# Kernel tuning notes

Hardware: AMD Instinct MI355X
Metric: run time of the kernel (lower is better)

## Reference

```python
import jax, jax.numpy as jnp
import numpy as np

B, TK, NK, H = 64, 512, 256, 512

def _masked_renorm_softmax(scores, mask):
    # softmax over last dim, multiply by mask, renormalize (as in the torch code)
    p = jax.nn.softmax(scores, axis=-1) * mask
    return p / jnp.sum(p, axis=-1, keepdims=True)

def setup_inputs() -> dict:
    key = jax.random.key(0)
    ks = jax.random.split(key, 14)
    s = 0.02
    return {
        "s_t_hat": jax.random.normal(ks[0], (B, 2 * H), jnp.float32),
        "encoder_outputs_token": jax.random.normal(ks[1], (B, TK, H), jnp.float32),
        "encoder_outputs_node": jax.random.normal(ks[2], (B, NK, H), jnp.float32),
        "node_to_token": jax.random.randint(ks[3], (B, TK), 0, NK),
        "enc_padding_mask_token": jnp.ones((B, TK), jnp.float32),
        "enc_padding_mask_node": jnp.ones((B, NK), jnp.float32),
        "graph": jax.random.uniform(ks[4], (B, NK, NK), jnp.float32),
        "flow": jax.random.uniform(ks[5], (B, NK), jnp.float32),
        # parameters (Linear weights stored as [in, out]; x @ W == torch Linear)
        "W_c": jax.random.normal(ks[6], (H,), jnp.float32) * s,          # Linear(1, H)
        "W_tok": jax.random.normal(ks[7], (H, H), jnp.float32) * s,      # encode_proj_token
        "W_node": jax.random.normal(ks[8], (H, H), jnp.float32) * s,     # encode_proj_node
        "W_dec": jax.random.normal(ks[9], (2 * H, H), jnp.float32) * s,  # decode_proj
        "b_dec": jnp.zeros((H,), jnp.float32),
        "v_tok": jax.random.normal(ks[10], (H,), jnp.float32) * s,       # v_token
        "v_node": jax.random.normal(ks[11], (H,), jnp.float32) * s,      # v_node
    }

def reference(s_t_hat, encoder_outputs_token, encoder_outputs_node, node_to_token,
              enc_padding_mask_token, enc_padding_mask_node, graph, flow,
              W_c, W_tok, W_node, W_dec, b_dec, v_tok, v_node):
    # projections
    enc_tok_feat = jnp.einsum('bth,hk->btk', encoder_outputs_token, W_tok)   # [B,TK,H]
    enc_node_feat = jnp.einsum('bnh,hk->bnk', encoder_outputs_node, W_node)  # [B,NK,H]
    dec_fea = s_t_hat @ W_dec + b_dec                                        # [B,H]
    flow_feat = flow[..., None] * W_c                                        # [B,NK,H]

    # node attention
    e_node = jnp.tanh(enc_node_feat + dec_fea[:, None, :] + flow_feat)
    scores_node = jnp.einsum('bnh,h->bn', e_node, v_node)                    # [B,NK]
    attn_dist_node = _masked_renorm_softmax(scores_node, enc_padding_mask_node)

    # gather node attention onto tokens via node_to_token indices
    gathered = jnp.take_along_axis(attn_dist_node, node_to_token, axis=1)    # [B,TK]
    attn_dist_node_to_token = _masked_renorm_softmax(gathered, enc_padding_mask_token)

    # token attention
    e_tok = jnp.tanh(enc_tok_feat + dec_fea[:, None, :])
    scores_tok = jnp.einsum('bth,h->bt', e_tok, v_tok)                       # [B,TK]
    attn_dist_token = _masked_renorm_softmax(scores_tok, enc_padding_mask_token)

    # mix and context
    final_attn = 0.5 * attn_dist_token + 0.5 * attn_dist_node_to_token      # [B,TK]
    c_t = jnp.einsum('bt,bth->bh', final_attn, encoder_outputs_token)        # [B,H]

    # multi-hop graph diffusion of node attention
    zero_hop = attn_dist_node                                                # [B,NK]
    one_hop = jnp.einsum('bn,bnm->bm', zero_hop, graph)
    two_hop = jnp.einsum('bn,bnm->bm', one_hop, graph)
    flow_out = (zero_hop + one_hop + two_hop) * 0.33333

    return (c_t, final_attn, attn_dist_node, flow_out)
```

## Files before the change

### kernel.cpp

```cpp
#include <hip/hip_runtime.h>
#include <math.h>

constexpr int kB = 64;
constexpr int kTK = 512;
constexpr int kNK = 256;
constexpr int kH = 512;
constexpr int kTokBlocks = kB * kTK / 64;
constexpr int kNodeBlocks = kB * kNK / 64;

typedef float f32x4 __attribute__((ext_vector_type(4)));
typedef __bf16 bf16x8 __attribute__((ext_vector_type(8)));

__device__ __forceinline__ unsigned short f32_to_bf16(float f) {
  return (unsigned short)((__float_as_uint(f) + 0x8000u) >> 16);
}

__device__ __forceinline__ float tanh_fast(float x) {
  float e = __builtin_amdgcn_exp2f(x * 2.8853900817779268f);
  return 1.0f - 2.0f * __builtin_amdgcn_rcpf(e + 1.0f);
}

__device__ __forceinline__ void lds_barrier() {
  __builtin_amdgcn_s_waitcnt(0xC07F);
  __builtin_amdgcn_s_barrier();
}

__device__ __forceinline__ void gload_lds16(const void* g, void* l) {
  __builtin_amdgcn_global_load_lds(
      (__attribute__((address_space(1))) void*)(g),
      (__attribute__((address_space(3))) void*)(l), 16, 0, 0);
}

__global__ __launch_bounds__(256) void prep_kernel(
    const float* __restrict__ Wtok, const float* __restrict__ Wnode,
    unsigned short* __restrict__ WtokT, unsigned short* __restrict__ WnodeT,
    const float* __restrict__ s_t_hat, const float* __restrict__ W_dec,
    float* __restrict__ dec_part) {
  __shared__ float sm[32 * 33];
  const int tid = threadIdx.x;
  if (blockIdx.x < 512) {
    const int idx = blockIdx.x;
    const int z = idx >> 8, rem = idx & 255;
    const int bx = rem & 15, by = rem >> 4;
    const float* W = z ? Wnode : Wtok;
    unsigned short* T = z ? WnodeT : WtokT;
    const int tx = tid & 31, ty = tid >> 5;
#pragma unroll
    for (int i = 0; i < 4; ++i)
      sm[(ty + 8 * i) * 33 + tx] =
          W[(size_t)(by * 32 + ty + 8 * i) * kH + bx * 32 + tx];
    __syncthreads();
#pragma unroll
    for (int i = 0; i < 4; ++i)
      T[(size_t)(bx * 32 + ty + 8 * i) * kH + by * 32 + tx] =
          f32_to_bf16(sm[tx * 33 + ty + 8 * i]);
  } else {
    const int r = blockIdx.x - 512;
    const int b = r >> 3, s = r & 7;
    if (tid < 128) sm[tid] = s_t_hat[(size_t)b * 1024 + s * 128 + tid];
    __syncthreads();
    float a0 = 0.f, a1 = 0.f;
    const float* w = W_dec + (size_t)(s * 128) * kH;
#pragma unroll 8
    for (int k = 0; k < 128; ++k) {
      a0 = fmaf(sm[k], w[(size_t)k * kH + tid], a0);
      a1 = fmaf(sm[k], w[(size_t)k * kH + tid + 256], a1);
    }
    dec_part[(size_t)(b * 8 + s) * kH + tid] = a0;
    dec_part[(size_t)(b * 8 + s) * kH + tid + 256] = a1;
  }
}

__global__ __launch_bounds__(512, 4) void scores_fused_kernel(
    const float* __restrict__ enc_tok, const float* __restrict__ enc_node,
    const unsigned short* __restrict__ WtokT,
    const unsigned short* __restrict__ WnodeT,
    const float* __restrict__ dec_part, const float* __restrict__ b_dec,
    const float* __restrict__ flow, const float* __restrict__ W_c,
    const float* __restrict__ v_tok, const float* __restrict__ v_node,
    float* __restrict__ scores_tok, float* __restrict__ scores_node) {
  const int tid = threadIdx.x;
  const int wave = tid >> 6, lane = tid & 63;
  const int quad = lane >> 4, l15 = lane & 15;
  const bool is_node = blockIdx.x >= kTokBlocks;
  const int bidx = is_node ? (int)blockIdx.x - kTokBlocks : (int)blockIdx.x;
  const float* A = is_node ? enc_node : enc_tok;
  const unsigned short* WT = is_node ? WnodeT : WtokT;
  const float* v = is_node ? v_node : v_tok;
  float* scores = is_node ? scores_node : scores_tok;
  const int ROWS = is_node ? kNK : kTK;
  const int b = is_node ? (bidx >> 2) : (bidx >> 3);
  const int row0 = (is_node ? (bidx & 3) : (bidx & 7)) * 64;

  __shared__ __align__(16) float fbuf[2][4096];
  __shared__ __align__(16) unsigned short hbuf[2][4096];
  __shared__ float red[8][64];

  const f32x4 fzero = {0.f, 0.f, 0.f, 0.f};
  f32x4 acc[4][4];
#pragma unroll
  for (int i = 0; i < 4; ++i)
#pragma unroll
    for (int j = 0; j < 4; ++j) acc[i][j] = fzero;

  const float* asrcw =
      A + (size_t)(b * ROWS + row0 + wave * 8 + (lane >> 4)) * kH + (lane & 15) * 4;
  auto stage = [&](int kc, int buf) {
    gload_lds16(asrcw + kc * 64, &fbuf[buf][(wave * 8) * 64]);
    gload_lds16(asrcw + 4 * kH + kc * 64, &fbuf[buf][(wave * 8 + 4) * 64]);
  };

  auto cvt = [&](int buf) {
#pragma unroll
    for (int j = 0; j < 2; ++j) {
      const int e0 = j * 2048 + tid * 4;
      const int row = e0 >> 6, k = e0 & 63;
      const f32x4 x = *(const f32x4*)&fbuf[buf][e0];
      ushort4 h;
      h.x = f32_to_bf16(x[0]); h.y = f32_to_bf16(x[1]);
      h.z = f32_to_bf16(x[2]); h.w = f32_to_bf16(x[3]);
      const int s16 = (k >> 3) ^ (row & 7);
      *(ushort4*)((char*)&hbuf[buf][0] + row * 128 + s16 * 16 + (k & 7) * 2) = h;
    }
  };

  auto readfrag = [&](int buf, int ks, int mi) {
    const int row = mi * 16 + l15;
    const int s16 = (ks * 4 + quad) ^ (row & 7);
    return *(const bf16x8*)((const char*)&hbuf[buf][0] + row * 128 + s16 * 16);
  };

  const int n0 = wave * 64;
  const unsigned short* bbase = WT + (size_t)(n0 + l15) * kH + quad * 8;
  bf16x8 bbuf[2][2];
  auto loadB = [&](int sb, int g, int half) {
    bbuf[sb][0] = *(const bf16x8*)(bbase + (size_t)(16 * (2 * half + 0)) * kH + g * 32);
    bbuf[sb][1] = *(const bf16x8*)(bbase + (size_t)(16 * (2 * half + 1)) * kH + g * 32);
  };

  stage(0, 0);
  loadB(0, 0, 0);
  loadB(1, 0, 1);

#pragma unroll
  for (int kc = 0; kc < 8; ++kc) {
    __builtin_amdgcn_s_waitcnt(0x0F70);
    __builtin_amdgcn_sched_barrier(0);
    cvt(kc & 1);
    if (kc < 7) stage(kc + 1, (kc + 1) & 1);
    lds_barrier();
#pragma unroll
    for (int ks = 0; ks < 2; ++ks) {
      const int g = kc * 2 + ks;
      bf16x8 afr[4];
#pragma unroll
      for (int mi = 0; mi < 4; ++mi) afr[mi] = readfrag(kc & 1, ks, mi);
      if (g > 0) loadB(1, g, 1);
      __builtin_amdgcn_s_setprio(1);
#pragma unroll
      for (int mi = 0; mi < 4; ++mi)
#pragma unroll
        for (int ni = 0; ni < 2; ++ni)
          acc[mi][ni] = __builtin_amdgcn_mfma_f32_16x16x32_bf16(
              afr[mi], bbuf[0][ni], acc[mi][ni], 0, 0, 0);
      __builtin_amdgcn_s_setprio(0);
      if (g < 15) loadB(0, g + 1, 0);
      __builtin_amdgcn_s_setprio(1);
#pragma unroll
      for (int mi = 0; mi < 4; ++mi)
#pragma unroll
        for (int ni = 0; ni < 2; ++ni)
          acc[mi][ni + 2] = __builtin_amdgcn_mfma_f32_16x16x32_bf16(
              afr[mi], bbuf[1][ni], acc[mi][ni + 2], 0, 0, 0);
      __builtin_amdgcn_s_setprio(0);
    }
  }

  float dec2[4], vv2[4], wc2[4];
#pragma unroll
  for (int ni = 0; ni < 4; ++ni) {
    const int col = n0 + 16 * ni + l15;
    float d = b_dec[col];
#pragma unroll
    for (int p = 0; p < 8; ++p) d += dec_part[(size_t)(b * 8 + p) * kH + col];
    dec2[ni] = d;
    vv2[ni] = v[col];
    wc2[ni] = is_node ? W_c[col] : 0.f;
  }
#pragma unroll
  for (int mi = 0; mi < 4; ++mi) {
#pragma unroll
    for (int reg = 0; reg < 4; ++reg) {
      const int row = 16 * mi + quad * 4 + reg;
      const float fl = is_node ? flow[b * kNK + row0 + row] : 0.f;
      float p = 0.f;
#pragma unroll
      for (int ni = 0; ni < 4; ++ni)
        p += tanh_fast(fmaf(fl, wc2[ni], acc[mi][ni][reg] + dec2[ni])) * vv2[ni];
#pragma unroll
      for (int off = 1; off < 16; off <<= 1) p += __shfl_xor(p, off, 64);
      if (l15 == 0) red[wave][row] = p;
    }
  }
  __syncthreads();
  if (tid < 64) {
    float s = 0.f;
#pragma unroll
    for (int w = 0; w < 8; ++w) s += red[w][tid];
    scores[b * ROWS + row0 + tid] = s;
  }
}

__device__ __forceinline__ float block_sum_512(float v, float* rbuf) {
#pragma unroll
  for (int off = 32; off >= 1; off >>= 1) v += __shfl_xor(v, off, 64);
  if ((threadIdx.x & 63) == 0) rbuf[threadIdx.x >> 6] = v;
  __syncthreads();
  float s = rbuf[0];
#pragma unroll
  for (int w = 1; w < 8; ++w) s += rbuf[w];
  __syncthreads();
  return s;
}

__global__ __launch_bounds__(512) void softmax_mix_kernel(
    const float* __restrict__ scores_node, const float* __restrict__ scores_tok,
    const int* __restrict__ node_to_token,
    const float* __restrict__ mask_tok, const float* __restrict__ mask_node,
    float* __restrict__ out_final, float* __restrict__ out_attn_node,
    float* __restrict__ out_flow) {
  const int b = blockIdx.x, tid = threadIdx.x;
  __shared__ float an_sh[kNK];
  __shared__ float rbuf[8];

  if (tid < kNK) out_flow[b * kNK + tid] = 0.f;

  float en = 0.f;
  if (tid < kNK)
    en = expf(scores_node[b * kNK + tid]) * mask_node[b * kNK + tid];
  float sn = block_sum_512(en, rbuf);
  float an = en / sn;
  if (tid < kNK) {
    an_sh[tid] = an;
    out_attn_node[b * kNK + tid] = an;
  }
  __syncthreads();

  const float mt = mask_tok[b * kTK + tid];
  const int idx = node_to_token[b * kTK + tid];
  float eg = expf(an_sh[idx]) * mt;
  float sg = block_sum_512(eg, rbuf);
  float an2t = eg / sg;

  float et = expf(scores_tok[b * kTK + tid]) * mt;
  float st = block_sum_512(et, rbuf);
  float at = et / st;

  out_final[b * kTK + tid] = 0.5f * (at + an2t);
}

__global__ __launch_bounds__(512) void ct_flow1_kernel(
    const float* __restrict__ final_attn, const float* __restrict__ enc_tok,
    const float* __restrict__ attn_node, const float* __restrict__ graph,
    float* __restrict__ ctp, float* __restrict__ fp1) {
  const int tid = threadIdx.x;
  if (blockIdx.x < 512) {
    const int b = blockIdx.x >> 3, s = blockIdx.x & 7;
    __shared__ float fa[64];
    __shared__ float part[4][512];
    if (tid < 64) fa[tid] = final_attn[b * kTK + s * 64 + tid];
    __syncthreads();
    const int h4 = (tid & 127) * 4, tsub = tid >> 7;
    float4 acc = {0.f, 0.f, 0.f, 0.f};
    const float* base =
        enc_tok + ((size_t)(b * kTK + s * 64 + tsub * 16)) * kH + h4;
#pragma unroll
    for (int t = 0; t < 16; ++t) {
      float4 e = *(const float4*)(base + (size_t)t * kH);
      const float w = fa[tsub * 16 + t];
      acc.x = fmaf(w, e.x, acc.x); acc.y = fmaf(w, e.y, acc.y);
      acc.z = fmaf(w, e.z, acc.z); acc.w = fmaf(w, e.w, acc.w);
    }
    *(float4*)&part[tsub][h4] = acc;
    __syncthreads();
    if (tid < 128) {
      float4 s0 = {0.f, 0.f, 0.f, 0.f};
#pragma unroll
      for (int p = 0; p < 4; ++p) {
        float4 pp = *(const float4*)&part[p][tid * 4];
        s0.x += pp.x; s0.y += pp.y; s0.z += pp.z; s0.w += pp.w;
      }
      *(float4*)&ctp[((size_t)(b * 8 + s)) * kH + tid * 4] = s0;
    }
  } else {
    const int rr = blockIdx.x - 512;
    const int b = rr >> 2, sl = rr & 3;
    __shared__ float z[64];
    __shared__ float part[8][256];
    if (tid < 64) z[tid] = attn_node[b * kNK + sl * 64 + tid];
    __syncthreads();
    const int m4 = (tid & 63) * 4, nsub = tid >> 6;
    float4 acc = {0.f, 0.f, 0.f, 0.f};
    const float* g =
        graph + ((size_t)(b * kNK + sl * 64 + nsub * 8)) * kNK + m4;
#pragma unroll
    for (int n = 0; n < 8; ++n) {
      float4 gg = *(const float4*)(g + (size_t)n * kNK);
      const float w = z[nsub * 8 + n];
      acc.x = fmaf(w, gg.x, acc.x); acc.y = fmaf(w, gg.y, acc.y);
      acc.z = fmaf(w, gg.z, acc.z); acc.w = fmaf(w, gg.w, acc.w);
    }
    *(float4*)&part[nsub][m4] = acc;
    __syncthreads();
    if (tid < 64) {
      float4 s0 = {0.f, 0.f, 0.f, 0.f};
#pragma unroll
      for (int p = 0; p < 8; ++p) {
        float4 pp = *(const float4*)&part[p][tid * 4];
        s0.x += pp.x; s0.y += pp.y; s0.z += pp.z; s0.w += pp.w;
      }
      *(float4*)&fp1[((size_t)(b * 4 + sl)) * kNK + tid * 4] = s0;
    }
  }
}

__global__ __launch_bounds__(512) void ct_flow2_kernel(
    const float* __restrict__ ctp, const float* __restrict__ fp1,
    const float* __restrict__ attn_node, const float* __restrict__ graph,
    float* __restrict__ out_ct, float* __restrict__ out_flow) {
  const int tid = threadIdx.x;
  if (blockIdx.x < 64) {
    const int b = blockIdx.x;
    __shared__ float acc_sh[4][512];
    const int h4 = (tid & 127) * 4, part = tid >> 7;
    float4 a = {0.f, 0.f, 0.f, 0.f};
#pragma unroll
    for (int j = 0; j < 2; ++j) {
      float4 c = *(const float4*)&ctp[((size_t)(b * 8 + part * 2 + j)) * kH + h4];
      a.x += c.x; a.y += c.y; a.z += c.z; a.w += c.w;
    }
    *(float4*)&acc_sh[part][h4] = a;
    __syncthreads();
    if (tid < 128) {
      float4 s = {0.f, 0.f, 0.f, 0.f};
#pragma unroll
      for (int p = 0; p < 4; ++p) {
        float4 pp = *(const float4*)&acc_sh[p][tid * 4];
        s.x += pp.x; s.y += pp.y; s.z += pp.z; s.w += pp.w;
      }
      *(float4*)&out_ct[b * kH + tid * 4] = s;
    }
  } else {
    const int rr = blockIdx.x - 64;
    const int b = rr >> 2, sl = rr & 3;
    __shared__ float one_sh[64];
    __shared__ float part2[8][256];
    if (tid < 64) {
      const int n = sl * 64 + tid;
      float one = 0.f;
#pragma unroll
      for (int p = 0; p < 4; ++p) one += fp1[((size_t)(b * 4 + p)) * kNK + n];
      one_sh[tid] = one;
      atomicAdd(&out_flow[b * kNK + n],
                (attn_node[b * kNK + n] + one) * 0.33333f);
    }
    __syncthreads();
    const int m4 = (tid & 63) * 4, nsub = tid >> 6;
    float4 acc = {0.f, 0.f, 0.f, 0.f};
    const float* g =
        graph + ((size_t)(b * kNK + sl * 64 + nsub * 8)) * kNK + m4;
#pragma unroll
    for (int n = 0; n < 8; ++n) {
      float4 gg = *(const float4*)(g + (size_t)n * kNK);
      const float w = one_sh[sl * 0 + nsub * 8 + n];
      acc.x = fmaf(w, gg.x, acc.x); acc.y = fmaf(w, gg.y, acc.y);
      acc.z = fmaf(w, gg.z, acc.z); acc.w = fmaf(w, gg.w, acc.w);
    }
    *(float4*)&part2[nsub][m4] = acc;
    __syncthreads();
    if (tid < 64) {
      float4 s = {0.f, 0.f, 0.f, 0.f};
#pragma unroll
      for (int p = 0; p < 8; ++p) {
        float4 pp = *(const float4*)&part2[p][tid * 4];
        s.x += pp.x; s.y += pp.y; s.z += pp.z; s.w += pp.w;
      }
      float* dst = &out_flow[b * kNK + tid * 4];
      atomicAdd(dst + 0, s.x * 0.33333f);
      atomicAdd(dst + 1, s.y * 0.33333f);
      atomicAdd(dst + 2, s.z * 0.33333f);
      atomicAdd(dst + 3, s.w * 0.33333f);
    }
  }
}

extern "C" void kernel_launch(void* const* d_in, const int* in_sizes, int n_in,
                              void* d_out, int out_size, void* d_ws, size_t ws_size,
                              hipStream_t stream) {
  (void)in_sizes; (void)n_in; (void)out_size; (void)ws_size;
  const float* s_t_hat  = (const float*)d_in[0];
  const float* enc_tok  = (const float*)d_in[1];
  const float* enc_node = (const float*)d_in[2];
  const int*   n2t      = (const int*)d_in[3];
  const float* mask_tok = (const float*)d_in[4];
  const float* mask_nd  = (const float*)d_in[5];
  const float* graph    = (const float*)d_in[6];
  const float* flow     = (const float*)d_in[7];
  const float* W_c      = (const float*)d_in[8];
  const float* W_tok    = (const float*)d_in[9];
  const float* W_node   = (const float*)d_in[10];
  const float* W_dec    = (const float*)d_in[11];
  const float* b_dec    = (const float*)d_in[12];
  const float* v_tok    = (const float*)d_in[13];
  const float* v_node   = (const float*)d_in[14];

  float* out = (float*)d_out;
  float* out_ct        = out;
  float* out_final     = out + kB * kH;
  float* out_attn_node = out + 2 * kB * kH;
  float* out_flow      = out_attn_node + kB * kNK;

  float* ws = (float*)d_ws;
  float* scores_tok  = ws;
  float* scores_node = ws + 32768;
  float* dec_part    = ws + 49152;
  float* ctp         = dec_part;
  float* fp1         = ws + 311296;
  unsigned short* WtokT  = (unsigned short*)(ws + 376832);
  unsigned short* WnodeT = WtokT + kH * kH;

  prep_kernel<<<1024, 256, 0, stream>>>(W_tok, W_node, WtokT, WnodeT,
                                        s_t_hat, W_dec, dec_part);
  scores_fused_kernel<<<kTokBlocks + kNodeBlocks, 512, 0, stream>>>(
      enc_tok, enc_node, WtokT, WnodeT, dec_part, b_dec, flow, W_c,
      v_tok, v_node, scores_tok, scores_node);
  softmax_mix_kernel<<<kB, 512, 0, stream>>>(scores_node, scores_tok, n2t,
                                             mask_tok, mask_nd, out_final,
                                             out_attn_node, out_flow);
  ct_flow1_kernel<<<768, 512, 0, stream>>>(out_final, enc_tok, out_attn_node,
                                           graph, ctp, fp1);
  ct_flow2_kernel<<<320, 512, 0, stream>>>(ctp, fp1, out_attn_node, graph,
                                           out_ct, out_flow);
}
```

Baseline: 235.9 us.

## Split scores GEMM across two column-half blocks with partial score sums

The fused scores kernel now launches twice as many 256-thread blocks, each covering half of the output columns (256 of 512) for a 64-row tile. Each block writes a partial score into a separate half of an enlarged scores buffer, and the softmax kernel adds the two partials before exponentiating. This raises block count and parallelism across CUs, and gives each wave 16 rows of the A staging instead of 8. The cost is that every A tile is loaded and converted to bf16 twice, and the workspace layout shifts to fit the doubled score buffers.

```diff
diff --git a/kernel.cpp b/kernel.cpp
--- a/kernel.cpp
+++ b/kernel.cpp
@@ -5,8 +5,6 @@
 constexpr int kTK = 512;
 constexpr int kNK = 256;
 constexpr int kH = 512;
-constexpr int kTokBlocks = kB * kTK / 64;
-constexpr int kNodeBlocks = kB * kNK / 64;
 
 typedef float f32x4 __attribute__((ext_vector_type(4)));
 typedef __bf16 bf16x8 __attribute__((ext_vector_type(8)));
@@ -71,7 +69,7 @@
   }
 }
 
-__global__ __launch_bounds__(512, 4) void scores_fused_kernel(
+__global__ __launch_bounds__(256, 3) void scores_fused_kernel(
     const float* __restrict__ enc_tok, const float* __restrict__ enc_node,
     const unsigned short* __restrict__ WtokT,
     const unsigned short* __restrict__ WnodeT,
@@ -82,19 +80,22 @@
   const int tid = threadIdx.x;
   const int wave = tid >> 6, lane = tid & 63;
   const int quad = lane >> 4, l15 = lane & 15;
-  const bool is_node = blockIdx.x >= kTokBlocks;
-  const int bidx = is_node ? (int)blockIdx.x - kTokBlocks : (int)blockIdx.x;
+  const bool is_node = blockIdx.x >= 1024;
+  int bx = is_node ? (int)blockIdx.x - 1024 : (int)blockIdx.x;
+  const int colhalf = bx & 1;
+  bx >>= 1;
   const float* A = is_node ? enc_node : enc_tok;
   const unsigned short* WT = is_node ? WnodeT : WtokT;
   const float* v = is_node ? v_node : v_tok;
-  float* scores = is_node ? scores_node : scores_tok;
   const int ROWS = is_node ? kNK : kTK;
-  const int b = is_node ? (bidx >> 2) : (bidx >> 3);
-  const int row0 = (is_node ? (bidx & 3) : (bidx & 7)) * 64;
+  const int b = is_node ? (bx >> 2) : (bx >> 3);
+  const int row0 = (is_node ? (bx & 3) : (bx & 7)) * 64;
+  float* scores = (is_node ? scores_node : scores_tok) +
+                  (size_t)colhalf * (kB * ROWS);
 
   __shared__ __align__(16) float fbuf[2][4096];
   __shared__ __align__(16) unsigned short hbuf[2][4096];
-  __shared__ float red[8][64];
+  __shared__ float red[4][64];
 
   const f32x4 fzero = {0.f, 0.f, 0.f, 0.f};
   f32x4 acc[4][4];
@@ -104,16 +105,18 @@
     for (int j = 0; j < 4; ++j) acc[i][j] = fzero;
 
   const float* asrcw =
-      A + (size_t)(b * ROWS + row0 + wave * 8 + (lane >> 4)) * kH + (lane & 15) * 4;
+      A + (size_t)(b * ROWS + row0 + wave * 16 + (lane >> 4)) * kH + (lane & 15) * 4;
   auto stage = [&](int kc, int buf) {
-    gload_lds16(asrcw + kc * 64, &fbuf[buf][(wave * 8) * 64]);
-    gload_lds16(asrcw + 4 * kH + kc * 64, &fbuf[buf][(wave * 8 + 4) * 64]);
+#pragma unroll
+    for (int j = 0; j < 4; ++j)
+      gload_lds16(asrcw + (size_t)(4 * j) * kH + kc * 64,
+                  &fbuf[buf][(wave * 16 + 4 * j) * 64]);
   };
 
   auto cvt = [&](int buf) {
 #pragma unroll
-    for (int j = 0; j < 2; ++j) {
-      const int e0 = j * 2048 + tid * 4;
+    for (int j = 0; j < 4; ++j) {
+      const int e0 = j * 1024 + tid * 4;
       const int row = e0 >> 6, k = e0 & 63;
       const f32x4 x = *(const f32x4*)&fbuf[buf][e0];
       ushort4 h;
@@ -130,7 +133,7 @@
     return *(const bf16x8*)((const char*)&hbuf[buf][0] + row * 128 + s16 * 16);
   };
 
-  const int n0 = wave * 64;
+  const int n0 = colhalf * 256 + wave * 64;
   const unsigned short* bbase = WT + (size_t)(n0 + l15) * kH + quad * 8;
   bf16x8 bbuf[2][2];
   auto loadB = [&](int sb, int g, int half) {
@@ -206,7 +209,7 @@
   if (tid < 64) {
     float s = 0.f;
 #pragma unroll
-    for (int w = 0; w < 8; ++w) s += red[w][tid];
+    for (int w = 0; w < 4; ++w) s += red[w][tid];
     scores[b * ROWS + row0 + tid] = s;
   }
 }
@@ -236,8 +239,11 @@
   if (tid < kNK) out_flow[b * kNK + tid] = 0.f;
 
   float en = 0.f;
-  if (tid < kNK)
-    en = expf(scores_node[b * kNK + tid]) * mask_node[b * kNK + tid];
+  if (tid < kNK) {
+    const float s2 = scores_node[b * kNK + tid] +
+                     scores_node[kB * kNK + b * kNK + tid];
+    en = expf(s2) * mask_node[b * kNK + tid];
+  }
   float sn = block_sum_512(en, rbuf);
   float an = en / sn;
   if (tid < kNK) {
@@ -252,7 +258,9 @@
   float sg = block_sum_512(eg, rbuf);
   float an2t = eg / sg;
 
-  float et = expf(scores_tok[b * kTK + tid]) * mt;
+  const float st2 = scores_tok[b * kTK + tid] +
+                    scores_tok[kB * kTK + b * kTK + tid];
+  float et = expf(st2) * mt;
   float st = block_sum_512(et, rbuf);
   float at = et / st;
 
@@ -422,16 +430,16 @@
 
   float* ws = (float*)d_ws;
   float* scores_tok  = ws;
-  float* scores_node = ws + 32768;
-  float* dec_part    = ws + 49152;
+  float* scores_node = ws + 65536;
+  float* dec_part    = ws + 98304;
   float* ctp         = dec_part;
-  float* fp1         = ws + 311296;
-  unsigned short* WtokT  = (unsigned short*)(ws + 376832);
+  float* fp1         = ws + 360448;
+  unsigned short* WtokT  = (unsigned short*)(ws + 425984);
   unsigned short* WnodeT = WtokT + kH * kH;
 
   prep_kernel<<<1024, 256, 0, stream>>>(W_tok, W_node, WtokT, WnodeT,
                                         s_t_hat, W_dec, dec_part);
-  scores_fused_kernel<<<kTokBlocks + kNodeBlocks, 512, 0, stream>>>(
+  scores_fused_kernel<<<1536, 256, 0, stream>>>(
       enc_tok, enc_node, WtokT, WnodeT, dec_part, b_dec, flow, W_c,
       v_tok, v_node, scores_tok, scores_node);
   softmax_mix_kernel<<<kB, 512, 0, stream>>>(scores_node, scores_tok, n2t,
```

Result: no change. 239.5 us (+1.5%).

## Triple-buffer A staging and burst-load B fragments per K chunk

Applied to the files above, without the earlier changes.

Raises the fp32 LDS staging of the A tile from double to triple buffering, so global-to-LDS loads are issued two chunks ahead and the wait keeps two loads in flight. The B weight fragments for a whole K chunk (8 fragments) are now loaded in one burst before the barrier instead of being interleaved between MFMA halves. The fp32-to-bf16 conversion is remapped so each thread converts 8 contiguous values and writes one 16-byte packed store. LDS use and register pressure both grow, so launch bounds drop from 4 to 3 blocks per CU, trading occupancy for deeper prefetch.

```diff
diff --git a/kernel.cpp b/kernel.cpp
--- a/kernel.cpp
+++ b/kernel.cpp
@@ -9,10 +9,15 @@
 constexpr int kNodeBlocks = kB * kNK / 64;
 
 typedef float f32x4 __attribute__((ext_vector_type(4)));
+typedef unsigned uint4v __attribute__((ext_vector_type(4)));
 typedef __bf16 bf16x8 __attribute__((ext_vector_type(8)));
 
 __device__ __forceinline__ unsigned short f32_to_bf16(float f) {
   return (unsigned short)((__float_as_uint(f) + 0x8000u) >> 16);
+}
+
+__device__ __forceinline__ unsigned pk_bf16x2(float lo, float hi) {
+  return (unsigned)f32_to_bf16(lo) | ((unsigned)f32_to_bf16(hi) << 16);
 }
 
 __device__ __forceinline__ float tanh_fast(float x) {
@@ -71,7 +76,7 @@
   }
 }
 
-__global__ __launch_bounds__(512, 4) void scores_fused_kernel(
+__global__ __launch_bounds__(512, 3) void scores_fused_kernel(
     const float* __restrict__ enc_tok, const float* __restrict__ enc_node,
     const unsigned short* __restrict__ WtokT,
     const unsigned short* __restrict__ WnodeT,
@@ -92,7 +97,7 @@
   const int b = is_node ? (bidx >> 2) : (bidx >> 3);
   const int row0 = (is_node ? (bidx & 3) : (bidx & 7)) * 64;
 
-  __shared__ __align__(16) float fbuf[2][4096];
+  __shared__ __align__(16) float fbuf[3][4096];
   __shared__ __align__(16) unsigned short hbuf[2][4096];
   __shared__ float red[8][64];
 
@@ -107,21 +112,21 @@
       A + (size_t)(b * ROWS + row0 + wave * 8 + (lane >> 4)) * kH + (lane & 15) * 4;
   auto stage = [&](int kc, int buf) {
     gload_lds16(asrcw + kc * 64, &fbuf[buf][(wave * 8) * 64]);
-    gload_lds16(asrcw + 4 * kH + kc * 64, &fbuf[buf][(wave * 8 + 4) * 64]);
+    gload_lds16(asrcw + (size_t)4 * kH + kc * 64, &fbuf[buf][(wave * 8 + 4) * 64]);
   };
 
-  auto cvt = [&](int buf) {
-#pragma unroll
-    for (int j = 0; j < 2; ++j) {
-      const int e0 = j * 2048 + tid * 4;
-      const int row = e0 >> 6, k = e0 & 63;
-      const f32x4 x = *(const f32x4*)&fbuf[buf][e0];
-      ushort4 h;
-      h.x = f32_to_bf16(x[0]); h.y = f32_to_bf16(x[1]);
-      h.z = f32_to_bf16(x[2]); h.w = f32_to_bf16(x[3]);
-      const int s16 = (k >> 3) ^ (row & 7);
-      *(ushort4*)((char*)&hbuf[buf][0] + row * 128 + s16 * 16 + (k & 7) * 2) = h;
-    }
+  const int crow = wave * 8 + (lane >> 3);
+  const int ck0 = (lane & 7) * 8;
+  const int cdst = crow * 128 + (((ck0 >> 3) ^ (crow & 7)) * 16);
+  auto cvt = [&](int fb, int hb) {
+    const f32x4 x0 = *(const f32x4*)&fbuf[fb][crow * 64 + ck0];
+    const f32x4 x1 = *(const f32x4*)&fbuf[fb][crow * 64 + ck0 + 4];
+    uint4v h;
+    h[0] = pk_bf16x2(x0[0], x0[1]);
+    h[1] = pk_bf16x2(x0[2], x0[3]);
+    h[2] = pk_bf16x2(x1[0], x1[1]);
+    h[3] = pk_bf16x2(x1[2], x1[3]);
+    *(uint4v*)((char*)&hbuf[hb][0] + cdst) = h;
   };
 
   auto readfrag = [&](int buf, int ks, int mi) {
@@ -132,46 +137,44 @@
 
   const int n0 = wave * 64;
   const unsigned short* bbase = WT + (size_t)(n0 + l15) * kH + quad * 8;
-  bf16x8 bbuf[2][2];
-  auto loadB = [&](int sb, int g, int half) {
-    bbuf[sb][0] = *(const bf16x8*)(bbase + (size_t)(16 * (2 * half + 0)) * kH + g * 32);
-    bbuf[sb][1] = *(const bf16x8*)(bbase + (size_t)(16 * (2 * half + 1)) * kH + g * 32);
+  bf16x8 bbuf[8];
+  auto loadBburst = [&](int kc) {
+#pragma unroll
+    for (int f = 0; f < 8; ++f) {
+      const int ks = f >> 2, ni = f & 3;
+      bbuf[f] = *(const bf16x8*)(bbase + (size_t)(16 * ni) * kH +
+                                 (kc * 2 + ks) * 32);
+    }
   };
 
   stage(0, 0);
-  loadB(0, 0, 0);
-  loadB(1, 0, 1);
+  stage(1, 1);
 
 #pragma unroll
   for (int kc = 0; kc < 8; ++kc) {
-    __builtin_amdgcn_s_waitcnt(0x0F70);
+    if (kc < 7) {
+      __builtin_amdgcn_s_waitcnt(0x0F72);
+    } else {
+      __builtin_amdgcn_s_waitcnt(0x0F70);
+    }
     __builtin_amdgcn_sched_barrier(0);
-    cvt(kc & 1);
-    if (kc < 7) stage(kc + 1, (kc + 1) & 1);
+    cvt(kc % 3, kc & 1);
+    loadBburst(kc);
+    __builtin_amdgcn_sched_barrier(0);
+    if (kc < 6) stage(kc + 2, (kc + 2) % 3);
     lds_barrier();
 #pragma unroll
     for (int ks = 0; ks < 2; ++ks) {
-      const int g = kc * 2 + ks;
       bf16x8 afr[4];
 #pragma unroll
       for (int mi = 0; mi < 4; ++mi) afr[mi] = readfrag(kc & 1, ks, mi);
-      if (g > 0) loadB(1, g, 1);
       __builtin_amdgcn_s_setprio(1);
 #pragma unroll
       for (int mi = 0; mi < 4; ++mi)
 #pragma unroll
-        for (int ni = 0; ni < 2; ++ni)
+        for (int ni = 0; ni < 4; ++ni)
           acc[mi][ni] = __builtin_amdgcn_mfma_f32_16x16x32_bf16(
-              afr[mi], bbuf[0][ni], acc[mi][ni], 0, 0, 0);
-      __builtin_amdgcn_s_setprio(0);
-      if (g < 15) loadB(0, g + 1, 0);
-      __builtin_amdgcn_s_setprio(1);
-#pragma unroll
-      for (int mi = 0; mi < 4; ++mi)
-#pragma unroll
-        for (int ni = 0; ni < 2; ++ni)
-          acc[mi][ni + 2] = __builtin_amdgcn_mfma_f32_16x16x32_bf16(
-              afr[mi], bbuf[1][ni], acc[mi][ni + 2], 0, 0, 0);
+              afr[mi], bbuf[ks * 4 + ni], acc[mi][ni], 0, 0, 0);
       __builtin_amdgcn_s_setprio(0);
     }
   }
```

Result: no change. 234.7 us (-0.5%).
